# Optimization experiments

Measured on AMD Instinct MI355X. Metric: run time of the kernel, lower is better.

The kernel has to match this reference:

```python
import jax, jax.numpy as jnp
import numpy as np

N_NODES = 50000
N_EDGES = 800000
IN_F = 512
OUT_F = 96
ALPHA = 0.1
ITERATIONS = 10
AVG_DEG = 16


def setup_inputs() -> dict:
    key = jax.random.key(0)
    k1, k2, k3, k4, k5 = jax.random.split(key, 5)
    x = jax.random.normal(k1, (N_NODES, IN_F), dtype=jnp.float32)
    # xavier_uniform with gain=1.414 over [IN_F, OUT_F]
    limit = 1.414 * np.sqrt(6.0 / (IN_F + OUT_F))
    weight = jax.random.uniform(k2, (IN_F, OUT_F), dtype=jnp.float32,
                                minval=-limit, maxval=limit)
    edge_src = jax.random.randint(k3, (N_EDGES,), 0, N_NODES, dtype=jnp.int32)
    edge_dst = jax.random.randint(k4, (N_EDGES,), 0, N_NODES, dtype=jnp.int32)
    # values scaled like a row-normalized adjacency for stable propagation
    edge_val = jax.random.uniform(k5, (N_EDGES,), dtype=jnp.float32) / AVG_DEG
    return {"x": x, "weight": weight, "edge_src": edge_src,
            "edge_dst": edge_dst, "edge_val": edge_val}


def _spmm(edge_src, edge_dst, edge_val, h):
    # out[i] = sum_{edges e with dst=i} val[e] * h[src[e]]
    gathered = h[edge_src] * edge_val[:, None]          # [E, OUT_F]
    return jax.ops.segment_sum(gathered, edge_dst, num_segments=N_NODES)


def reference(x, weight, edge_src, edge_dst, edge_val):
    support = x @ weight                                 # [N, OUT_F]
    prev = support
    def body(_, s):
        s = _spmm(edge_src, edge_dst, edge_val, s) * (1.0 - ALPHA) + prev * ALPHA
        return jax.nn.relu(s)
    return jax.lax.fori_loop(0, ITERATIONS, body, support)
```

## Files before the change

kernel.cpp:

```cpp
#include <hip/hip_runtime.h>

typedef unsigned int  uint;
typedef unsigned short ushort;

#define N_NODES 50000
#define N_EDGES 800000
#define IN_F    512
#define OUT_F   96

__device__ __forceinline__ float bflo(uint u) { return __uint_as_float(u << 16); }
__device__ __forceinline__ float bfhi(uint u) { return __uint_as_float(u & 0xffff0000u); }
__device__ __forceinline__ uint f2bf(float x) {
    uint u = __float_as_uint(x);
    return (u + 0x7fffu + ((u >> 16) & 1u)) >> 16;
}
__device__ __forceinline__ uint pack2bf(float lo, float hi) {
    return f2bf(lo) | (f2bf(hi) << 16);
}

__global__ __launch_bounds__(256) void gemm_kernel(const float* __restrict__ x,
                                                   const float* __restrict__ w,
                                                   ushort* __restrict__ supB) {
    __shared__ float xs[32][68];
    __shared__ float wsh[32 * 96];
    const int tid  = threadIdx.x;
    const int row0 = blockIdx.x * 64;
    const int tr = tid >> 4;
    const int tc = tid & 15;
    const int r0 = tr * 4;
    const int c0 = tc * 6;

    float acc[4][6];
    #pragma unroll
    for (int i = 0; i < 4; ++i)
        #pragma unroll
        for (int j = 0; j < 6; ++j) acc[i][j] = 0.f;

    const int lr  = tid >> 2;
    const int lk4 = (tid & 3) * 4;
    const int grow = row0 + lr;

    for (int k0 = 0; k0 < IN_F; k0 += 32) {
        #pragma unroll
        for (int hh = 0; hh < 2; ++hh) {
            int kk = lk4 + 16 * hh;
            float4 xv = make_float4(0.f, 0.f, 0.f, 0.f);
            if (grow < N_NODES)
                xv = *(const float4*)(x + (size_t)grow * IN_F + k0 + kk);
            xs[kk + 0][lr] = xv.x; xs[kk + 1][lr] = xv.y;
            xs[kk + 2][lr] = xv.z; xs[kk + 3][lr] = xv.w;
        }
        const float4* wsrc = (const float4*)(w + (size_t)k0 * OUT_F);
        #pragma unroll
        for (int j = 0; j < 3; ++j)
            ((float4*)wsh)[tid + 256 * j] = wsrc[tid + 256 * j];
        __syncthreads();
        #pragma unroll
        for (int kk = 0; kk < 32; ++kk) {
            float4 a = *(const float4*)&xs[kk][r0];
            const float* bp = &wsh[kk * 96 + c0];
            float b[6];
            *(float2*)&b[0] = *(const float2*)(bp + 0);
            *(float2*)&b[2] = *(const float2*)(bp + 2);
            *(float2*)&b[4] = *(const float2*)(bp + 4);
            #pragma unroll
            for (int j = 0; j < 6; ++j) {
                acc[0][j] = fmaf(a.x, b[j], acc[0][j]);
                acc[1][j] = fmaf(a.y, b[j], acc[1][j]);
                acc[2][j] = fmaf(a.z, b[j], acc[2][j]);
                acc[3][j] = fmaf(a.w, b[j], acc[3][j]);
            }
        }
        __syncthreads();
    }
    #pragma unroll
    for (int i = 0; i < 4; ++i) {
        int gr = row0 + r0 + i;
        if (gr < N_NODES) {
            uint* p = (uint*)(supB + (size_t)gr * OUT_F + c0);
            p[0] = pack2bf(acc[i][0], acc[i][1]);
            p[1] = pack2bf(acc[i][2], acc[i][3]);
            p[2] = pack2bf(acc[i][4], acc[i][5]);
        }
    }
}

#define SCAN_BLOCKS 196

__global__ void zero_kernel(int* __restrict__ p, int n) {
    int t = blockIdx.x * blockDim.x + threadIdx.x;
    if (t < n) p[t] = 0;
}

__global__ void hist_kernel(const int* __restrict__ dst, int* __restrict__ counts) {
    int e = blockIdx.x * blockDim.x + threadIdx.x;
    if (e < N_EDGES) atomicAdd(&counts[dst[e]], 1);
}

__global__ __launch_bounds__(256) void block_reduce_kernel(const int* __restrict__ counts,
                                                           int* __restrict__ blockSums) {
    __shared__ int s[256];
    int idx = blockIdx.x * 256 + threadIdx.x;
    s[threadIdx.x] = (idx < N_NODES) ? counts[idx] : 0;
    __syncthreads();
    for (int off = 128; off > 0; off >>= 1) {
        if (threadIdx.x < off) s[threadIdx.x] += s[threadIdx.x + off];
        __syncthreads();
    }
    if (threadIdx.x == 0) blockSums[blockIdx.x] = s[0];
}

__global__ __launch_bounds__(256) void scan_sums_kernel(int* __restrict__ blockSums,
                                                        int* __restrict__ blockOffs,
                                                        int* __restrict__ rowstart) {
    __shared__ int s[256];
    int t = threadIdx.x;
    s[t] = (t < SCAN_BLOCKS) ? blockSums[t] : 0;
    __syncthreads();
    for (int off = 1; off < 256; off <<= 1) {
        int v = (t >= off) ? s[t - off] : 0;
        __syncthreads();
        s[t] += v;
        __syncthreads();
    }
    if (t < SCAN_BLOCKS) blockOffs[t] = (t == 0) ? 0 : s[t - 1];
    if (t == 0) rowstart[N_NODES] = s[SCAN_BLOCKS - 1];
}

__global__ __launch_bounds__(256) void block_scan_kernel(const int* __restrict__ counts,
                                                         const int* __restrict__ blockOffs,
                                                         int* __restrict__ rowstart,
                                                         int* __restrict__ cursor) {
    __shared__ int s[256];
    int t   = threadIdx.x;
    int idx = blockIdx.x * 256 + t;
    int v   = (idx < N_NODES) ? counts[idx] : 0;
    s[t] = v;
    __syncthreads();
    for (int off = 1; off < 256; off <<= 1) {
        int u = (t >= off) ? s[t - off] : 0;
        __syncthreads();
        s[t] += u;
        __syncthreads();
    }
    if (idx < N_NODES) {
        int excl = blockOffs[blockIdx.x] + s[t] - v;
        rowstart[idx] = excl;
        cursor[idx]   = excl;
    }
}

__global__ void scatter_kernel(const int* __restrict__ src, const int* __restrict__ dst,
                               const float* __restrict__ val, int* __restrict__ cursor,
                               int2* __restrict__ edgeP) {
    int e = blockIdx.x * blockDim.x + threadIdx.x;
    if (e < N_EDGES) {
        int d   = dst[e];
        int pos = atomicAdd(&cursor[d], 1);
        edgeP[pos] = make_int2(src[e], __float_as_int(val[e]));
    }
}

#define TPN 24

template <bool FINAL>
__global__ __launch_bounds__(256) void prop_kernel(const ushort* __restrict__ h,
                                                   const ushort* __restrict__ supB,
                                                   const int* __restrict__ rowstart,
                                                   const int2* __restrict__ edgeP,
                                                   ushort* __restrict__ outB,
                                                   float* __restrict__ outF) {
    int t = blockIdx.x * blockDim.x + threadIdx.x;
    int i = t / TPN;
    if (i >= N_NODES) return;
    int q = t - i * TPN;
    int f = q * 4;

    int start = rowstart[i];
    int end   = rowstart[i + 1];

    float a0 = 0.f, a1 = 0.f, a2 = 0.f, a3 = 0.f;
    int e = start;
    for (; e + 1 < end; e += 2) {
        int2 e0 = edgeP[e];
        int2 e1 = edgeP[e + 1];
        float v0 = __int_as_float(e0.y);
        float v1 = __int_as_float(e1.y);
        uint2 h0 = *(const uint2*)(h + (size_t)e0.x * OUT_F + f);
        uint2 h1 = *(const uint2*)(h + (size_t)e1.x * OUT_F + f);
        a0 = fmaf(v0, bflo(h0.x), a0); a1 = fmaf(v0, bfhi(h0.x), a1);
        a2 = fmaf(v0, bflo(h0.y), a2); a3 = fmaf(v0, bfhi(h0.y), a3);
        a0 = fmaf(v1, bflo(h1.x), a0); a1 = fmaf(v1, bfhi(h1.x), a1);
        a2 = fmaf(v1, bflo(h1.y), a2); a3 = fmaf(v1, bfhi(h1.y), a3);
    }
    if (e < end) {
        int2 e0 = edgeP[e];
        float v0 = __int_as_float(e0.y);
        uint2 h0 = *(const uint2*)(h + (size_t)e0.x * OUT_F + f);
        a0 = fmaf(v0, bflo(h0.x), a0); a1 = fmaf(v0, bfhi(h0.x), a1);
        a2 = fmaf(v0, bflo(h0.y), a2); a3 = fmaf(v0, bfhi(h0.y), a3);
    }

    size_t o = (size_t)i * OUT_F + f;
    uint2 sp = *(const uint2*)(supB + o);
    float r0 = fmaxf(fmaf(a0, 0.9f, bflo(sp.x) * 0.1f), 0.f);
    float r1 = fmaxf(fmaf(a1, 0.9f, bfhi(sp.x) * 0.1f), 0.f);
    float r2 = fmaxf(fmaf(a2, 0.9f, bflo(sp.y) * 0.1f), 0.f);
    float r3 = fmaxf(fmaf(a3, 0.9f, bfhi(sp.y) * 0.1f), 0.f);

    if (FINAL) {
        *(float4*)(outF + o) = make_float4(r0, r1, r2, r3);
    } else {
        *(uint2*)(outB + o) = make_uint2(pack2bf(r0, r1), pack2bf(r2, r3));
    }
}

extern "C" void kernel_launch(void* const* d_in, const int* in_sizes, int n_in,
                              void* d_out, int out_size, void* d_ws, size_t ws_size,
                              hipStream_t stream) {
    const float* x    = (const float*)d_in[0];
    const float* w    = (const float*)d_in[1];
    const int*   esrc = (const int*)d_in[2];
    const int*   edst = (const int*)d_in[3];
    const float* eval = (const float*)d_in[4];
    float* out = (float*)d_out;

    char*  xb  = (char*)d_in[0];
    size_t off = 0;
    auto alloc = [&](size_t bytes) -> char* {
        char* p = xb + off;
        off = (off + bytes + 255) & ~(size_t)255;
        return p;
    };
    ushort* supB      = (ushort*)alloc((size_t)N_NODES * OUT_F * sizeof(ushort));
    ushort* hU        = (ushort*)alloc((size_t)N_NODES * OUT_F * sizeof(ushort));
    ushort* hV        = (ushort*)alloc((size_t)N_NODES * OUT_F * sizeof(ushort));
    int2*   edgeP     = (int2*)alloc((size_t)N_EDGES * sizeof(int2));
    int*    rowstart  = (int*)alloc((N_NODES + 1) * sizeof(int));
    int*    cursor    = (int*)alloc(N_NODES * sizeof(int));
    int*    counts    = (int*)alloc(N_NODES * sizeof(int));
    int*    blockSums = (int*)alloc(SCAN_BLOCKS * sizeof(int));
    int*    blockOffs = (int*)alloc(SCAN_BLOCKS * sizeof(int));

    gemm_kernel<<<(N_NODES + 63) / 64, 256, 0, stream>>>(x, w, supB);

    zero_kernel<<<(N_NODES + 255) / 256, 256, 0, stream>>>(counts, N_NODES);
    hist_kernel<<<(N_EDGES + 255) / 256, 256, 0, stream>>>(edst, counts);
    block_reduce_kernel<<<SCAN_BLOCKS, 256, 0, stream>>>(counts, blockSums);
    scan_sums_kernel<<<1, 256, 0, stream>>>(blockSums, blockOffs, rowstart);
    block_scan_kernel<<<SCAN_BLOCKS, 256, 0, stream>>>(counts, blockOffs,
                                                       rowstart, cursor);
    scatter_kernel<<<(N_EDGES + 255) / 256, 256, 0, stream>>>(esrc, edst, eval,
                                                              cursor, edgeP);

    const int pthreads = N_NODES * TPN;
    const int pgrid    = (pthreads + 255) / 256;
    const ushort* in = supB;
    for (int it = 1; it <= 9; ++it) {
        ushort* o = (it & 1) ? hU : hV;
        prop_kernel<false><<<pgrid, 256, 0, stream>>>(in, supB, rowstart, edgeP,
                                                      o, nullptr);
        in = o;
    }
    prop_kernel<true><<<pgrid, 256, 0, stream>>>(in, supB, rowstart, edgeP,
                                                 nullptr, out);
}
```

Baseline: 648.5 us.

## Use bf16 MFMA for projection GEMM and widen SpMM to 8 features per thread

Replaces the fp32 shared-memory GEMM with a bf16 MFMA kernel. A small kernel pre-transposes the weight to bf16, and x is converted to bf16 on the fly. The propagation kernel now handles 8 features per thread with 16-byte gathers and unrolls over 4 edges, cutting thread count and index loads. Scratch buffers are placed in the output buffer, and an extra device copy of the support matrix is added. The bf16 rounding of x adds some precision loss.

```diff
diff --git a/kernel.cpp b/kernel.cpp
--- a/kernel.cpp
+++ b/kernel.cpp
@@ -1,12 +1,16 @@
 #include <hip/hip_runtime.h>
 
-typedef unsigned int  uint;
+typedef unsigned int   uint;
 typedef unsigned short ushort;
+typedef __attribute__((ext_vector_type(8))) short bf16x8;
+typedef __attribute__((ext_vector_type(4))) float f32x4;
 
 #define N_NODES 50000
 #define N_EDGES 800000
 #define IN_F    512
 #define OUT_F   96
+#define SCAN_BLOCKS 196
+#define TPN 12
 
 __device__ __forceinline__ float bflo(uint u) { return __uint_as_float(u << 16); }
 __device__ __forceinline__ float bfhi(uint u) { return __uint_as_float(u & 0xffff0000u); }
@@ -18,74 +22,58 @@
     return f2bf(lo) | (f2bf(hi) << 16);
 }
 
+__global__ __launch_bounds__(256) void wt_kernel(const float* __restrict__ w,
+                                                 ushort* __restrict__ wT) {
+    int t = blockIdx.x * 256 + threadIdx.x;
+    if (t < IN_F * OUT_F) {
+        int k = t / OUT_F, c = t - k * OUT_F;
+        wT[(size_t)c * IN_F + k] = (ushort)f2bf(w[t]);
+    }
+}
+
 __global__ __launch_bounds__(256) void gemm_kernel(const float* __restrict__ x,
-                                                   const float* __restrict__ w,
+                                                   const ushort* __restrict__ wT,
                                                    ushort* __restrict__ supB) {
-    __shared__ float xs[32][68];
-    __shared__ float wsh[32 * 96];
     const int tid  = threadIdx.x;
-    const int row0 = blockIdx.x * 64;
-    const int tr = tid >> 4;
-    const int tc = tid & 15;
-    const int r0 = tr * 4;
-    const int c0 = tc * 6;
-
-    float acc[4][6];
+    const int wv   = tid >> 6;
+    const int lane = tid & 63;
+    const int m    = lane & 15;
+    const int quad = lane >> 4;
+
+    const int row  = blockIdx.x * 64 + wv * 16 + m;
+    const int arow = (row < N_NODES) ? row : (N_NODES - 1);
+    const float* xp = x + (size_t)arow * IN_F + quad * 8;
+
+    f32x4 acc[6];
     #pragma unroll
-    for (int i = 0; i < 4; ++i)
+    for (int ct = 0; ct < 6; ++ct) acc[ct] = (f32x4){0.f, 0.f, 0.f, 0.f};
+
+    for (int k0 = 0; k0 < IN_F; k0 += 32) {
+        float4 xa = *(const float4*)(xp + k0);
+        float4 xb = *(const float4*)(xp + k0 + 4);
+        union { uint u[4]; bf16x8 v; } af;
+        af.u[0] = pack2bf(xa.x, xa.y); af.u[1] = pack2bf(xa.z, xa.w);
+        af.u[2] = pack2bf(xb.x, xb.y); af.u[3] = pack2bf(xb.z, xb.w);
         #pragma unroll
-        for (int j = 0; j < 6; ++j) acc[i][j] = 0.f;
-
-    const int lr  = tid >> 2;
-    const int lk4 = (tid & 3) * 4;
-    const int grow = row0 + lr;
-
-    for (int k0 = 0; k0 < IN_F; k0 += 32) {
+        for (int ct = 0; ct < 6; ++ct) {
+            bf16x8 bf = *(const bf16x8*)(wT + (size_t)(ct * 16 + m) * IN_F
+                                            + k0 + quad * 8);
+            acc[ct] = __builtin_amdgcn_mfma_f32_16x16x32_bf16(af.v, bf, acc[ct],
+                                                              0, 0, 0);
+        }
+    }
+
+    const int orow0 = blockIdx.x * 64 + wv * 16 + quad * 4;
+    #pragma unroll
+    for (int ct = 0; ct < 6; ++ct) {
         #pragma unroll
-        for (int hh = 0; hh < 2; ++hh) {
-            int kk = lk4 + 16 * hh;
-            float4 xv = make_float4(0.f, 0.f, 0.f, 0.f);
-            if (grow < N_NODES)
-                xv = *(const float4*)(x + (size_t)grow * IN_F + k0 + kk);
-            xs[kk + 0][lr] = xv.x; xs[kk + 1][lr] = xv.y;
-            xs[kk + 2][lr] = xv.z; xs[kk + 3][lr] = xv.w;
+        for (int r = 0; r < 4; ++r) {
+            int gr = orow0 + r;
+            if (gr < N_NODES)
+                supB[(size_t)gr * OUT_F + ct * 16 + m] = (ushort)f2bf(acc[ct][r]);
         }
-        const float4* wsrc = (const float4*)(w + (size_t)k0 * OUT_F);
-        #pragma unroll
-        for (int j = 0; j < 3; ++j)
-            ((float4*)wsh)[tid + 256 * j] = wsrc[tid + 256 * j];
-        __syncthreads();
-        #pragma unroll
-        for (int kk = 0; kk < 32; ++kk) {
-            float4 a = *(const float4*)&xs[kk][r0];
-            const float* bp = &wsh[kk * 96 + c0];
-            float b[6];
-            *(float2*)&b[0] = *(const float2*)(bp + 0);
-            *(float2*)&b[2] = *(const float2*)(bp + 2);
-            *(float2*)&b[4] = *(const float2*)(bp + 4);
-            #pragma unroll
-            for (int j = 0; j < 6; ++j) {
-                acc[0][j] = fmaf(a.x, b[j], acc[0][j]);
-                acc[1][j] = fmaf(a.y, b[j], acc[1][j]);
-                acc[2][j] = fmaf(a.z, b[j], acc[2][j]);
-                acc[3][j] = fmaf(a.w, b[j], acc[3][j]);
-            }
-        }
-        __syncthreads();
-    }
-    #pragma unroll
-    for (int i = 0; i < 4; ++i) {
-        int gr = row0 + r0 + i;
-        if (gr < N_NODES) {
-            uint* p = (uint*)(supB + (size_t)gr * OUT_F + c0);
-            p[0] = pack2bf(acc[i][0], acc[i][1]);
-            p[1] = pack2bf(acc[i][2], acc[i][3]);
-            p[2] = pack2bf(acc[i][4], acc[i][5]);
-        }
-    }
-}
-
-#define SCAN_BLOCKS 196
+    }
+}
 
 __global__ void zero_kernel(int* __restrict__ p, int n) {
     int t = blockIdx.x * blockDim.x + threadIdx.x;
@@ -161,57 +149,69 @@
     }
 }
 
-#define TPN 24
+__device__ __forceinline__ void acc8(float* a, float v, uint4 hv) {
+    a[0] = fmaf(v, bflo(hv.x), a[0]); a[1] = fmaf(v, bfhi(hv.x), a[1]);
+    a[2] = fmaf(v, bflo(hv.y), a[2]); a[3] = fmaf(v, bfhi(hv.y), a[3]);
+    a[4] = fmaf(v, bflo(hv.z), a[4]); a[5] = fmaf(v, bfhi(hv.z), a[5]);
+    a[6] = fmaf(v, bflo(hv.w), a[6]); a[7] = fmaf(v, bfhi(hv.w), a[7]);
+}
 
 template <bool FINAL>
 __global__ __launch_bounds__(256) void prop_kernel(const ushort* __restrict__ h,
-                                                   const ushort* __restrict__ supB,
+                                                   const ushort* __restrict__ sup,
                                                    const int* __restrict__ rowstart,
                                                    const int2* __restrict__ edgeP,
                                                    ushort* __restrict__ outB,
                                                    float* __restrict__ outF) {
-    int t = blockIdx.x * blockDim.x + threadIdx.x;
+    int t = blockIdx.x * 256 + threadIdx.x;
     int i = t / TPN;
     if (i >= N_NODES) return;
     int q = t - i * TPN;
-    int f = q * 4;
+    int f = q * 8;
 
     int start = rowstart[i];
     int end   = rowstart[i + 1];
 
-    float a0 = 0.f, a1 = 0.f, a2 = 0.f, a3 = 0.f;
+    float a[8] = {0.f, 0.f, 0.f, 0.f, 0.f, 0.f, 0.f, 0.f};
     int e = start;
-    for (; e + 1 < end; e += 2) {
+    for (; e + 3 < end; e += 4) {
         int2 e0 = edgeP[e];
         int2 e1 = edgeP[e + 1];
-        float v0 = __int_as_float(e0.y);
-        float v1 = __int_as_float(e1.y);
-        uint2 h0 = *(const uint2*)(h + (size_t)e0.x * OUT_F + f);
-        uint2 h1 = *(const uint2*)(h + (size_t)e1.x * OUT_F + f);
-        a0 = fmaf(v0, bflo(h0.x), a0); a1 = fmaf(v0, bfhi(h0.x), a1);
-        a2 = fmaf(v0, bflo(h0.y), a2); a3 = fmaf(v0, bfhi(h0.y), a3);
-        a0 = fmaf(v1, bflo(h1.x), a0); a1 = fmaf(v1, bfhi(h1.x), a1);
-        a2 = fmaf(v1, bflo(h1.y), a2); a3 = fmaf(v1, bfhi(h1.y), a3);
-    }
-    if (e < end) {
+        int2 e2 = edgeP[e + 2];
+        int2 e3 = edgeP[e + 3];
+        uint4 h0 = *(const uint4*)(h + (size_t)e0.x * OUT_F + f);
+        uint4 h1 = *(const uint4*)(h + (size_t)e1.x * OUT_F + f);
+        uint4 h2 = *(const uint4*)(h + (size_t)e2.x * OUT_F + f);
+        uint4 h3 = *(const uint4*)(h + (size_t)e3.x * OUT_F + f);
+        acc8(a, __int_as_float(e0.y), h0);
+        acc8(a, __int_as_float(e1.y), h1);
+        acc8(a, __int_as_float(e2.y), h2);
+        acc8(a, __int_as_float(e3.y), h3);
+    }
+    for (; e < end; ++e) {
         int2 e0 = edgeP[e];
-        float v0 = __int_as_float(e0.y);
-        uint2 h0 = *(const uint2*)(h + (size_t)e0.x * OUT_F + f);
-        a0 = fmaf(v0, bflo(h0.x), a0); a1 = fmaf(v0, bfhi(h0.x), a1);
-        a2 = fmaf(v0, bflo(h0.y), a2); a3 = fmaf(v0, bfhi(h0.y), a3);
+        uint4 h0 = *(const uint4*)(h + (size_t)e0.x * OUT_F + f);
+        acc8(a, __int_as_float(e0.y), h0);
     }
 
     size_t o = (size_t)i * OUT_F + f;
-    uint2 sp = *(const uint2*)(supB + o);
-    float r0 = fmaxf(fmaf(a0, 0.9f, bflo(sp.x) * 0.1f), 0.f);
-    float r1 = fmaxf(fmaf(a1, 0.9f, bfhi(sp.x) * 0.1f), 0.f);
-    float r2 = fmaxf(fmaf(a2, 0.9f, bflo(sp.y) * 0.1f), 0.f);
-    float r3 = fmaxf(fmaf(a3, 0.9f, bfhi(sp.y) * 0.1f), 0.f);
+    uint4 sp = *(const uint4*)(sup + o);
+    float r[8];
+    r[0] = fmaxf(fmaf(a[0], 0.9f, bflo(sp.x) * 0.1f), 0.f);
+    r[1] = fmaxf(fmaf(a[1], 0.9f, bfhi(sp.x) * 0.1f), 0.f);
+    r[2] = fmaxf(fmaf(a[2], 0.9f, bflo(sp.y) * 0.1f), 0.f);
+    r[3] = fmaxf(fmaf(a[3], 0.9f, bfhi(sp.y) * 0.1f), 0.f);
+    r[4] = fmaxf(fmaf(a[4], 0.9f, bflo(sp.z) * 0.1f), 0.f);
+    r[5] = fmaxf(fmaf(a[5], 0.9f, bfhi(sp.z) * 0.1f), 0.f);
+    r[6] = fmaxf(fmaf(a[6], 0.9f, bflo(sp.w) * 0.1f), 0.f);
+    r[7] = fmaxf(fmaf(a[7], 0.9f, bfhi(sp.w) * 0.1f), 0.f);
 
     if (FINAL) {
-        *(float4*)(outF + o) = make_float4(r0, r1, r2, r3);
+        *(float4*)(outF + o)     = make_float4(r[0], r[1], r[2], r[3]);
+        *(float4*)(outF + o + 4) = make_float4(r[4], r[5], r[6], r[7]);
     } else {
-        *(uint2*)(outB + o) = make_uint2(pack2bf(r0, r1), pack2bf(r2, r3));
+        *(uint4*)(outB + o) = make_uint4(pack2bf(r[0], r[1]), pack2bf(r[2], r[3]),
+                                         pack2bf(r[4], r[5]), pack2bf(r[6], r[7]));
     }
 }
 
@@ -225,6 +225,11 @@
     const float* eval = (const float*)d_in[4];
     float* out = (float*)d_out;
 
+    const size_t supBytes = (size_t)N_NODES * OUT_F * sizeof(ushort);
+    ushort* supB = (ushort*)d_out;
+    ushort* wTb  = (ushort*)((char*)d_out + (size_t)out_size * 4
+                             - (size_t)IN_F * OUT_F * sizeof(ushort));
+
     char*  xb  = (char*)d_in[0];
     size_t off = 0;
     auto alloc = [&](size_t bytes) -> char* {
@@ -232,9 +237,9 @@
         off = (off + bytes + 255) & ~(size_t)255;
         return p;
     };
-    ushort* supB      = (ushort*)alloc((size_t)N_NODES * OUT_F * sizeof(ushort));
-    ushort* hU        = (ushort*)alloc((size_t)N_NODES * OUT_F * sizeof(ushort));
-    ushort* hV        = (ushort*)alloc((size_t)N_NODES * OUT_F * sizeof(ushort));
+    ushort* supB2     = (ushort*)alloc(supBytes);
+    ushort* hU        = (ushort*)alloc(supBytes);
+    ushort* hV        = (ushort*)alloc(supBytes);
     int2*   edgeP     = (int2*)alloc((size_t)N_EDGES * sizeof(int2));
     int*    rowstart  = (int*)alloc((N_NODES + 1) * sizeof(int));
     int*    cursor    = (int*)alloc(N_NODES * sizeof(int));
@@ -242,7 +247,11 @@
     int*    blockSums = (int*)alloc(SCAN_BLOCKS * sizeof(int));
     int*    blockOffs = (int*)alloc(SCAN_BLOCKS * sizeof(int));
 
-    gemm_kernel<<<(N_NODES + 63) / 64, 256, 0, stream>>>(x, w, supB);
+    wt_kernel<<<(IN_F * OUT_F + 255) / 256, 256, 0, stream>>>(w, wTb);
+
+    gemm_kernel<<<(N_NODES + 63) / 64, 256, 0, stream>>>(x, wTb, supB);
+
+    hipMemcpyAsync(supB2, supB, supBytes, hipMemcpyDeviceToDevice, stream);
 
     zero_kernel<<<(N_NODES + 255) / 256, 256, 0, stream>>>(counts, N_NODES);
     hist_kernel<<<(N_EDGES + 255) / 256, 256, 0, stream>>>(edst, counts);
@@ -253,15 +262,14 @@
     scatter_kernel<<<(N_EDGES + 255) / 256, 256, 0, stream>>>(esrc, edst, eval,
                                                               cursor, edgeP);
 
-    const int pthreads = N_NODES * TPN;
-    const int pgrid    = (pthreads + 255) / 256;
-    const ushort* in = supB;
+    const int pgrid = (N_NODES * TPN + 255) / 256;
+    const ushort* in = supB2;
     for (int it = 1; it <= 9; ++it) {
         ushort* o = (it & 1) ? hU : hV;
-        prop_kernel<false><<<pgrid, 256, 0, stream>>>(in, supB, rowstart, edgeP,
+        prop_kernel<false><<<pgrid, 256, 0, stream>>>(in, supB2, rowstart, edgeP,
                                                       o, nullptr);
         in = o;
     }
-    prop_kernel<true><<<pgrid, 256, 0, stream>>>(in, supB, rowstart, edgeP,
+    prop_kernel<true><<<pgrid, 256, 0, stream>>>(in, supB2, rowstart, edgeP,
                                                  nullptr, out);
 }
```

After: 562.3 us. -13.3%, faster.
